# Kernel tuning notes

Hardware: AMD Instinct MI355X
Metric: run time of the kernel (lower is better)

The kernel has to match this reference:

```python
import jax, jax.numpy as jnp
import numpy as np

DIM = 1024
N_HEADS = 16
HEAD_DIM = DIM // N_HEADS
MLP = 4 * DIM
B, N = 2, 2048
LN_EPS = 1e-5


def setup_inputs() -> dict:
    key = jax.random.key(0)
    ks = jax.random.split(key, 12)
    s = lambda fan_in: 1.0 / np.sqrt(fan_in)
    return {
        "x": jax.random.normal(ks[0], (B, N, DIM), dtype=jnp.float32),
        "qkv_w": jax.random.uniform(ks[1], (3 * DIM, DIM), jnp.float32, -s(DIM), s(DIM)),
        "out_w": jax.random.uniform(ks[2], (DIM, DIM), jnp.float32, -s(DIM), s(DIM)),
        "out_b": jax.random.uniform(ks[3], (DIM,), jnp.float32, -s(DIM), s(DIM)),
        "ff_w1": jax.random.uniform(ks[4], (MLP, DIM), jnp.float32, -s(DIM), s(DIM)),
        "ff_b1": jax.random.uniform(ks[5], (MLP,), jnp.float32, -s(DIM), s(DIM)),
        "ff_w2": jax.random.uniform(ks[6], (DIM, MLP), jnp.float32, -s(MLP), s(MLP)),
        "ff_b2": jax.random.uniform(ks[7], (DIM,), jnp.float32, -s(MLP), s(MLP)),
        "ln1_w": jnp.ones((DIM,), jnp.float32),
        "ln1_b": jnp.zeros((DIM,), jnp.float32),
        "ln2_w": jnp.ones((DIM,), jnp.float32),
        "ln2_b": jnp.zeros((DIM,), jnp.float32),
    }


def _layernorm(x, w, b):
    mu = jnp.mean(x, axis=-1, keepdims=True)
    var = jnp.mean(jnp.square(x - mu), axis=-1, keepdims=True)
    return (x - mu) * jax.lax.rsqrt(var + LN_EPS) * w + b


def reference(x, qkv_w, out_w, out_b, ff_w1, ff_b1, ff_w2, ff_b2,
              ln1_w, ln1_b, ln2_w, ln2_b):
    Bx, Nx, D = x.shape
    scale = HEAD_DIM ** -0.5
    x_ln = _layernorm(x, ln1_w, ln1_b)
    qkv = (x_ln @ qkv_w.T).reshape(Bx, Nx, 3, N_HEADS, HEAD_DIM)
    qkv = jnp.transpose(qkv, (2, 0, 3, 1, 4))  # [3, B, H, N, hd]
    q, k, v = qkv[0], qkv[1], qkv[2]
    attn = jnp.einsum('bhid,bhjd->bhij', q, k) * scale
    attn = jax.nn.softmax(attn, axis=-1)
    o = jnp.einsum('bhij,bhjd->bhid', attn, v)
    o = jnp.transpose(o, (0, 2, 1, 3)).reshape(Bx, Nx, D)
    x = x + o @ out_w.T + out_b
    x_ln2 = _layernorm(x, ln2_w, ln2_b)
    h = jax.nn.silu(x_ln2 @ ff_w1.T + ff_b1)
    x = x + h @ ff_w2.T + ff_b2
    return x
```

## Files before the change

### kernel.cpp

```cpp
#include <hip/hip_runtime.h>
#include <stdint.h>

#define DIM   1024
#define NH    16
#define HD    64
#define SEQ   2048
#define BATCH 2
#define MROWS 4096
#define MLPD  4096
#define LN_EPS 1e-5f
#define QSCALE 0.18033688011112042f

typedef _Float16 f16;
typedef _Float16 half8 __attribute__((ext_vector_type(8)));
typedef _Float16 half4 __attribute__((ext_vector_type(4)));
typedef float f32x4 __attribute__((ext_vector_type(4)));

__device__ __forceinline__ void async_cp16(const void* g, void* l) {
  __builtin_amdgcn_global_load_lds(
      (const __attribute__((address_space(1))) unsigned int*)g,
      (__attribute__((address_space(3))) unsigned int*)l, 16, 0, 0);
}

__global__ __launch_bounds__(256) void cvt_all_kernel(
    const float* __restrict__ w0, const float* __restrict__ w1,
    const float* __restrict__ w2, const float* __restrict__ w3,
    f16* __restrict__ d0, f16* __restrict__ d1, f16* __restrict__ d2,
    f16* __restrict__ d3) {
  int blk = blockIdx.x;
  const float* s;
  f16* d;
  int base;
  if (blk < 3072)      { s = w0; d = d0; base = blk; }
  else if (blk < 4096) { s = w1; d = d1; base = blk - 3072; }
  else if (blk < 8192) { s = w2; d = d2; base = blk - 4096; }
  else                 { s = w3; d = d3; base = blk - 8192; }
  int i = (base * 256 + threadIdx.x) * 4;
  float4 v = *(const float4*)(s + i);
  half4 o = { (f16)v.x, (f16)v.y, (f16)v.z, (f16)v.w };
  *(half4*)(d + i) = o;
}

__global__ __launch_bounds__(256) void ln_kernel(const float* __restrict__ x,
    const float* __restrict__ w, const float* __restrict__ b, f16* __restrict__ out) {
  __shared__ float red[8];
  int row = blockIdx.x, t = threadIdx.x;
  const float4 v = ((const float4*)(x + (size_t)row * DIM))[t];
  float s1 = v.x + v.y + v.z + v.w;
  float s2 = v.x * v.x + v.y * v.y + v.z * v.z + v.w * v.w;
#pragma unroll
  for (int m = 32; m; m >>= 1) { s1 += __shfl_xor(s1, m); s2 += __shfl_xor(s2, m); }
  if ((t & 63) == 0) { red[t >> 6] = s1; red[4 + (t >> 6)] = s2; }
  __syncthreads();
  s1 = red[0] + red[1] + red[2] + red[3];
  s2 = red[4] + red[5] + red[6] + red[7];
  float mu = s1 * (1.f / DIM);
  float rs = rsqrtf(s2 * (1.f / DIM) - mu * mu + LN_EPS);
  float4 wv = ((const float4*)w)[t];
  float4 bv = ((const float4*)b)[t];
  half4 o = { (f16)((v.x - mu) * rs * wv.x + bv.x), (f16)((v.y - mu) * rs * wv.y + bv.y),
              (f16)((v.z - mu) * rs * wv.z + bv.z), (f16)((v.w - mu) * rs * wv.w + bv.w) };
  ((half4*)(out + (size_t)row * DIM))[t] = o;
}

template <int MODE, int TN>
__global__ __launch_bounds__(256) void gemm_bt(
    const f16* __restrict__ A, const f16* __restrict__ W,
    const float* __restrict__ bias, const float* __restrict__ resid,
    float* __restrict__ outf, f16* __restrict__ outq, f16* __restrict__ outk,
    f16* __restrict__ outv, int K) {
  constexpr int IT = (TN == 128) ? 4 : 2;
  constexpr int MSUB = IT * 16;
  __shared__ __align__(16) f16 As[128 * 64];
  __shared__ __align__(16) f16 Bs[TN * 64];
  const int t = threadIdx.x;
  const int wave = t >> 6, lane = t & 63;
  const int n16 = lane & 15, quad = lane >> 4;
  const int tile_m = blockIdx.y * 128, tile_n = blockIdx.x * TN;
  const int wm = (TN == 128) ? (wave >> 1) : wave;
  const int wn = (TN == 128) ? (wave & 1) : 0;
  const int srow = lane >> 3, spos = lane & 7;
  const f32x4 zero4 = {0.f, 0.f, 0.f, 0.f};

  f32x4 acc[IT][4];
#pragma unroll
  for (int i = 0; i < IT; i++)
#pragma unroll
    for (int j = 0; j < 4; j++) acc[i][j] = zero4;

  for (int k0 = 0; k0 < K; k0 += 64) {
#pragma unroll
    for (int q = 0; q < 4; q++) {
      int r = q * 32 + wave * 8 + srow;
      int c = spos ^ (r & 7);
      async_cp16(A + (size_t)(tile_m + r) * K + k0 + c * 8, &As[q * 2048 + wave * 512]);
    }
#pragma unroll
    for (int q = 0; q < TN / 32; q++) {
      int r = q * 32 + wave * 8 + srow;
      int c = spos ^ (r & 7);
      async_cp16(W + (size_t)(tile_n + r) * K + k0 + c * 8, &Bs[q * 2048 + wave * 512]);
    }
    __syncthreads();
#pragma unroll
    for (int kk = 0; kk < 2; kk++) {
      half8 af[IT], bfr[4];
#pragma unroll
      for (int i = 0; i < IT; i++) {
        int row = wm * MSUB + i * 16 + n16;
        int c = (kk * 4 + quad) ^ (row & 7);
        af[i] = *(const half8*)&As[row * 64 + c * 8];
      }
#pragma unroll
      for (int j = 0; j < 4; j++) {
        int row = wn * 64 + j * 16 + n16;
        int c = (kk * 4 + quad) ^ (row & 7);
        bfr[j] = *(const half8*)&Bs[row * 64 + c * 8];
      }
#pragma unroll
      for (int i = 0; i < IT; i++)
#pragma unroll
        for (int j = 0; j < 4; j++)
          acc[i][j] = __builtin_amdgcn_mfma_f32_16x16x32_f16(af[i], bfr[j], acc[i][j], 0, 0, 0);
    }
    __syncthreads();
  }

#pragma unroll
  for (int i = 0; i < IT; i++) {
#pragma unroll
    for (int j = 0; j < 4; j++) {
      int gcol = tile_n + wn * 64 + j * 16 + n16;
      int grow0 = tile_m + wm * MSUB + i * 16 + quad * 4;
      if constexpr (MODE == 0) {
        int tsel = gcol >> 10, h = (gcol >> 6) & 15, d = gcol & 63;
        int bb = grow0 >> 11, nn0 = grow0 & 2047;
        if (tsel == 2) {
          half4 o;
#pragma unroll
          for (int r = 0; r < 4; r++) o[r] = (f16)acc[i][j][r];
          *(half4*)&outv[(((size_t)bb * NH + h) * HD + d) * SEQ + nn0] = o;
        } else {
          f16* dst = (tsel == 0) ? outq : outk;
          float sc = (tsel == 0) ? QSCALE : 1.0f;
#pragma unroll
          for (int r = 0; r < 4; r++)
            dst[(((size_t)bb * NH + h) * SEQ + nn0 + r) * HD + d] = (f16)(acc[i][j][r] * sc);
        }
      } else if constexpr (MODE == 1) {
#pragma unroll
        for (int r = 0; r < 4; r++) {
          size_t idx = (size_t)(grow0 + r) * DIM + gcol;
          outf[idx] = acc[i][j][r] + bias[gcol] + resid[idx];
        }
      } else {
#pragma unroll
        for (int r = 0; r < 4; r++) {
          float z = acc[i][j][r] + bias[gcol];
          float sg = 1.f / (1.f + __expf(-z));
          outq[(size_t)(grow0 + r) * MLPD + gcol] = (f16)(z * sg);
        }
      }
    }
  }
}

__global__ __launch_bounds__(256) void attn_kernel(const f16* __restrict__ qg,
    const f16* __restrict__ kg, const f16* __restrict__ vtg, f16* __restrict__ og) {
  __shared__ __align__(16) f16 Ks[64 * 64];
  __shared__ __align__(16) f16 Vs[64 * 64];
  const int bh = blockIdx.y, q0 = blockIdx.x * 64;
  const int t = threadIdx.x, wave = t >> 6, lane = t & 63;
  const int n16 = lane & 15, quad = lane >> 4;
  const int srow = lane >> 3, spos = lane & 7;
  const f32x4 zero4 = {0.f, 0.f, 0.f, 0.f};

  half8 qf0, qf1;
  {
    const f16* qr = qg + ((size_t)bh * SEQ + q0 + wave * 16 + n16) * HD + quad * 8;
    qf0 = *(const half8*)qr;
    qf1 = *(const half8*)(qr + 32);
  }

  f32x4 oc[4];
#pragma unroll
  for (int dt = 0; dt < 4; dt++) oc[dt] = zero4;
  float ls = 0.f;

  for (int kt64 = 0; kt64 < SEQ / 64; kt64++) {
    const int kv0 = kt64 * 64;
#pragma unroll
    for (int p = 0; p < 2; p++) {
      int r = p * 32 + wave * 8 + srow;
      int c = spos ^ (r & 7);
      async_cp16(kg + ((size_t)bh * SEQ + kv0 + r) * HD + c * 8, &Ks[p * 2048 + wave * 512]);
      async_cp16(vtg + ((size_t)bh * HD + r) * SEQ + kv0 + c * 8, &Vs[p * 2048 + wave * 512]);
    }
    __syncthreads();

    half4 pf[4];
#pragma unroll
    for (int kt = 0; kt < 4; kt++) {
      int row = kt * 16 + n16;
      half8 kf0 = *(const half8*)&Ks[row * 64 + (quad ^ (row & 7)) * 8];
      half8 kf1 = *(const half8*)&Ks[row * 64 + ((quad + 4) ^ (row & 7)) * 8];
      f32x4 z = zero4;
      z = __builtin_amdgcn_mfma_f32_16x16x32_f16(kf0, qf0, z, 0, 0, 0);
      z = __builtin_amdgcn_mfma_f32_16x16x32_f16(kf1, qf1, z, 0, 0, 0);
      half4 p4;
#pragma unroll
      for (int r = 0; r < 4; r++) {
        float p = __builtin_exp2f(z[r]);
        ls += p;
        p4[r] = (f16)p;
      }
      pf[kt] = p4;
    }

#pragma unroll
    for (int kt = 0; kt < 4; kt++) {
      half4 va[4];
#pragma unroll
      for (int dt = 0; dt < 4; dt++) {
        int row = dt * 16 + n16;
        int phys = (kt * 2 + (quad >> 1)) ^ (row & 7);
        va[dt] = *(const half4*)&Vs[row * 64 + phys * 8 + (quad & 1) * 4];
      }
#pragma unroll
      for (int dt = 0; dt < 4; dt++)
        oc[dt] = __builtin_amdgcn_mfma_f32_16x16x16f16(va[dt], pf[kt], oc[dt], 0, 0, 0);
    }
    __syncthreads();
  }

  ls += __shfl_xor(ls, 16);
  ls += __shfl_xor(ls, 32);
  float inv = 1.f / ls;
  const int b = bh >> 4, h = bh & 15;
#pragma unroll
  for (int dt = 0; dt < 4; dt++) {
    half4 o;
#pragma unroll
    for (int r = 0; r < 4; r++) o[r] = (f16)(oc[dt][r] * inv);
    *(half4*)&og[((size_t)b * SEQ + q0 + wave * 16 + n16) * DIM + h * HD + dt * 16 + quad * 4] = o;
  }
}

extern "C" void kernel_launch(void* const* d_in, const int* in_sizes, int n_in,
                              void* d_out, int out_size, void* d_ws, size_t ws_size,
                              hipStream_t stream) {
  const float* x     = (const float*)d_in[0];
  const float* qkv_w = (const float*)d_in[1];
  const float* out_w = (const float*)d_in[2];
  const float* out_b = (const float*)d_in[3];
  const float* ff_w1 = (const float*)d_in[4];
  const float* ff_b1 = (const float*)d_in[5];
  const float* ff_w2 = (const float*)d_in[6];
  const float* ff_b2 = (const float*)d_in[7];
  const float* ln1_w = (const float*)d_in[8];
  const float* ln1_b = (const float*)d_in[9];
  const float* ln2_w = (const float*)d_in[10];
  const float* ln2_b = (const float*)d_in[11];
  float* out = (float*)d_out;

  char* p = (char*)d_ws;
  size_t off = 0;
  auto alloc = [&](size_t bytes) {
    void* r = p + off;
    off += (bytes + 255) & ~(size_t)255;
    return r;
  };
  f16* wqkv = (f16*)alloc((size_t)3 * DIM * DIM * 2);
  f16* wout = (f16*)alloc((size_t)DIM * DIM * 2);
  f16* wf1  = (f16*)alloc((size_t)MLPD * DIM * 2);
  f16* wf2  = (f16*)alloc((size_t)MLPD * DIM * 2);
  f16* xln  = (f16*)alloc((size_t)MROWS * DIM * 2);
  f16* qb   = (f16*)alloc((size_t)MROWS * DIM * 2);
  f16* kb   = (f16*)alloc((size_t)MROWS * DIM * 2);
  f16* vtb  = (f16*)alloc((size_t)MROWS * DIM * 2);
  f16* obuf = (f16*)alloc((size_t)MROWS * DIM * 2);
  float* x1 = (float*)alloc((size_t)MROWS * DIM * 4);
  f16* hbuf = (f16*)alloc((size_t)MROWS * MLPD * 2);
  f16* x1ln = xln;

  cvt_all_kernel<<<12288, 256, 0, stream>>>(qkv_w, out_w, ff_w1, ff_w2,
                                            wqkv, wout, wf1, wf2);
  ln_kernel<<<MROWS, 256, 0, stream>>>(x, ln1_w, ln1_b, xln);
  gemm_bt<0, 128><<<dim3(3 * DIM / 128, MROWS / 128), 256, 0, stream>>>(
      xln, wqkv, nullptr, nullptr, nullptr, qb, kb, vtb, DIM);
  attn_kernel<<<dim3(SEQ / 64, BATCH * NH), 256, 0, stream>>>(qb, kb, vtb, obuf);
  gemm_bt<1, 64><<<dim3(DIM / 64, MROWS / 128), 256, 0, stream>>>(
      obuf, wout, out_b, x, x1, nullptr, nullptr, nullptr, DIM);
  ln_kernel<<<MROWS, 256, 0, stream>>>(x1, ln2_w, ln2_b, x1ln);
  gemm_bt<2, 128><<<dim3(MLPD / 128, MROWS / 128), 256, 0, stream>>>(
      x1ln, wf1, ff_b1, nullptr, nullptr, hbuf, nullptr, nullptr, DIM);
  gemm_bt<1, 64><<<dim3(DIM / 64, MROWS / 128), 256, 0, stream>>>(
      hbuf, wf2, ff_b2, x1, out, nullptr, nullptr, nullptr, MLPD);
}
```

Before: 368.7 us.

## Split attention over KV halves with 128-query tiles and a reduction kernel

Each attention block now handles 128 queries, two 16-row query tiles per wave, so every K/V tile loaded into shared memory is reused across twice as many queries. The key sequence is split into two 1024-key chunks along a new grid dimension. Each chunk writes unnormalized fp32 partial outputs and row sums into a scratch area that reuses the MLP hidden buffer, and a new reduce kernel combines the halves and normalizes to fp16. The aim is less K/V load and sync overhead per query while keeping the same block count, at the cost of extra fp32 partial traffic, a second launch and higher register pressure. The partials are summed without max subtraction, which matches the before code's use of exp2 without a running max.

```diff
diff --git a/kernel.cpp b/kernel.cpp
--- a/kernel.cpp
+++ b/kernel.cpp
@@ -165,30 +165,34 @@
   }
 }
 
-__global__ __launch_bounds__(256) void attn_kernel(const f16* __restrict__ qg,
-    const f16* __restrict__ kg, const f16* __restrict__ vtg, f16* __restrict__ og) {
+__global__ __launch_bounds__(256, 4) void attn_kernel(const f16* __restrict__ qg,
+    const f16* __restrict__ kg, const f16* __restrict__ vtg,
+    float* __restrict__ op, float* __restrict__ lp) {
   __shared__ __align__(16) f16 Ks[64 * 64];
   __shared__ __align__(16) f16 Vs[64 * 64];
-  const int bh = blockIdx.y, q0 = blockIdx.x * 64;
+  const int bh = blockIdx.z, kc = blockIdx.y, q0 = blockIdx.x * 128;
   const int t = threadIdx.x, wave = t >> 6, lane = t & 63;
   const int n16 = lane & 15, quad = lane >> 4;
   const int srow = lane >> 3, spos = lane & 7;
   const f32x4 zero4 = {0.f, 0.f, 0.f, 0.f};
 
-  half8 qf0, qf1;
-  {
-    const f16* qr = qg + ((size_t)bh * SEQ + q0 + wave * 16 + n16) * HD + quad * 8;
-    qf0 = *(const half8*)qr;
-    qf1 = *(const half8*)(qr + 32);
-  }
-
-  f32x4 oc[4];
-#pragma unroll
-  for (int dt = 0; dt < 4; dt++) oc[dt] = zero4;
-  float ls = 0.f;
-
-  for (int kt64 = 0; kt64 < SEQ / 64; kt64++) {
-    const int kv0 = kt64 * 64;
+  half8 qf[2][2];
+#pragma unroll
+  for (int qt = 0; qt < 2; qt++) {
+    const f16* qr = qg + ((size_t)bh * SEQ + q0 + wave * 32 + qt * 16 + n16) * HD + quad * 8;
+    qf[qt][0] = *(const half8*)qr;
+    qf[qt][1] = *(const half8*)(qr + 32);
+  }
+
+  f32x4 oc[2][4];
+#pragma unroll
+  for (int qt = 0; qt < 2; qt++)
+#pragma unroll
+    for (int dt = 0; dt < 4; dt++) oc[qt][dt] = zero4;
+  float ls[2] = {0.f, 0.f};
+
+  for (int kt64 = 0; kt64 < 16; kt64++) {
+    const int kv0 = kc * 1024 + kt64 * 64;
 #pragma unroll
     for (int p = 0; p < 2; p++) {
       int r = p * 32 + wave * 8 + srow;
@@ -198,24 +202,35 @@
     }
     __syncthreads();
 
-    half4 pf[4];
+    f32x4 st[4][2];
 #pragma unroll
     for (int kt = 0; kt < 4; kt++) {
       int row = kt * 16 + n16;
       half8 kf0 = *(const half8*)&Ks[row * 64 + (quad ^ (row & 7)) * 8];
       half8 kf1 = *(const half8*)&Ks[row * 64 + ((quad + 4) ^ (row & 7)) * 8];
-      f32x4 z = zero4;
-      z = __builtin_amdgcn_mfma_f32_16x16x32_f16(kf0, qf0, z, 0, 0, 0);
-      z = __builtin_amdgcn_mfma_f32_16x16x32_f16(kf1, qf1, z, 0, 0, 0);
-      half4 p4;
-#pragma unroll
-      for (int r = 0; r < 4; r++) {
-        float p = __builtin_exp2f(z[r]);
-        ls += p;
-        p4[r] = (f16)p;
-      }
-      pf[kt] = p4;
-    }
+#pragma unroll
+      for (int qt = 0; qt < 2; qt++) {
+        f32x4 z = zero4;
+        z = __builtin_amdgcn_mfma_f32_16x16x32_f16(kf0, qf[qt][0], z, 0, 0, 0);
+        z = __builtin_amdgcn_mfma_f32_16x16x32_f16(kf1, qf[qt][1], z, 0, 0, 0);
+        st[kt][qt] = z;
+      }
+    }
+
+    half4 pf[2][4];
+#pragma unroll
+    for (int qt = 0; qt < 2; qt++)
+#pragma unroll
+      for (int kt = 0; kt < 4; kt++) {
+        half4 p4;
+        float s0 = __builtin_exp2f(st[kt][qt][0]);
+        float s1 = __builtin_exp2f(st[kt][qt][1]);
+        float s2 = __builtin_exp2f(st[kt][qt][2]);
+        float s3 = __builtin_exp2f(st[kt][qt][3]);
+        p4[0] = (f16)s0; p4[1] = (f16)s1; p4[2] = (f16)s2; p4[3] = (f16)s3;
+        ls[qt] += (s0 + s1) + (s2 + s3);
+        pf[qt][kt] = p4;
+      }
 
 #pragma unroll
     for (int kt = 0; kt < 4; kt++) {
@@ -228,22 +243,43 @@
       }
 #pragma unroll
       for (int dt = 0; dt < 4; dt++)
-        oc[dt] = __builtin_amdgcn_mfma_f32_16x16x16f16(va[dt], pf[kt], oc[dt], 0, 0, 0);
+#pragma unroll
+        for (int qt = 0; qt < 2; qt++)
+          oc[qt][dt] = __builtin_amdgcn_mfma_f32_16x16x16f16(va[dt], pf[qt][kt], oc[qt][dt], 0, 0, 0);
     }
     __syncthreads();
   }
 
-  ls += __shfl_xor(ls, 16);
-  ls += __shfl_xor(ls, 32);
-  float inv = 1.f / ls;
   const int b = bh >> 4, h = bh & 15;
 #pragma unroll
-  for (int dt = 0; dt < 4; dt++) {
-    half4 o;
-#pragma unroll
-    for (int r = 0; r < 4; r++) o[r] = (f16)(oc[dt][r] * inv);
-    *(half4*)&og[((size_t)b * SEQ + q0 + wave * 16 + n16) * DIM + h * HD + dt * 16 + quad * 4] = o;
-  }
+  for (int qt = 0; qt < 2; qt++) {
+    float l = ls[qt];
+    l += __shfl_xor(l, 16);
+    l += __shfl_xor(l, 32);
+    int q = q0 + wave * 32 + qt * 16 + n16;
+    int row = b * SEQ + q;
+#pragma unroll
+    for (int dt = 0; dt < 4; dt++)
+      *(f32x4*)&op[((size_t)kc * MROWS + row) * DIM + h * HD + dt * 16 + quad * 4] = oc[qt][dt];
+    if (quad == 0) lp[((size_t)kc * BATCH * NH + bh) * SEQ + q] = l;
+  }
+}
+
+__global__ __launch_bounds__(256) void attn_reduce_kernel(const float* __restrict__ op,
+    const float* __restrict__ lp, f16* __restrict__ obuf) {
+  int row = blockIdx.x;
+  int t = threadIdx.x;
+  int b = row >> 11, q = row & 2047;
+  int h = t >> 4;
+  size_t base = (size_t)row * DIM + t * 4;
+  float4 o1 = *(const float4*)&op[base];
+  float4 o2 = *(const float4*)&op[(size_t)MROWS * DIM + base];
+  size_t li = ((size_t)b * NH + h) * SEQ + q;
+  float l = lp[li] + lp[(size_t)BATCH * NH * SEQ + li];
+  float inv = 1.f / l;
+  half4 o = { (f16)((o1.x + o2.x) * inv), (f16)((o1.y + o2.y) * inv),
+              (f16)((o1.z + o2.z) * inv), (f16)((o1.w + o2.w) * inv) };
+  *(half4*)&obuf[base] = o;
 }
 
 extern "C" void kernel_launch(void* const* d_in, const int* in_sizes, int n_in,
@@ -281,14 +317,17 @@
   f16* obuf = (f16*)alloc((size_t)MROWS * DIM * 2);
   float* x1 = (float*)alloc((size_t)MROWS * DIM * 4);
   f16* hbuf = (f16*)alloc((size_t)MROWS * MLPD * 2);
+  float* lp = (float*)alloc((size_t)2 * BATCH * NH * SEQ * 4);
   f16* x1ln = xln;
+  float* op = (float*)hbuf;
 
   cvt_all_kernel<<<12288, 256, 0, stream>>>(qkv_w, out_w, ff_w1, ff_w2,
                                             wqkv, wout, wf1, wf2);
   ln_kernel<<<MROWS, 256, 0, stream>>>(x, ln1_w, ln1_b, xln);
   gemm_bt<0, 128><<<dim3(3 * DIM / 128, MROWS / 128), 256, 0, stream>>>(
       xln, wqkv, nullptr, nullptr, nullptr, qb, kb, vtb, DIM);
-  attn_kernel<<<dim3(SEQ / 64, BATCH * NH), 256, 0, stream>>>(qb, kb, vtb, obuf);
+  attn_kernel<<<dim3(SEQ / 128, 2, BATCH * NH), 256, 0, stream>>>(qb, kb, vtb, op, lp);
+  attn_reduce_kernel<<<MROWS, 256, 0, stream>>>(op, lp, obuf);
   gemm_bt<1, 64><<<dim3(DIM / 64, MROWS / 128), 256, 0, stream>>>(
       obuf, wout, out_b, x, x1, nullptr, nullptr, nullptr, DIM);
   ln_kernel<<<MROWS, 256, 0, stream>>>(x1, ln2_w, ln2_b, x1ln);
```

After: 364.5 us. No clear change (-1.1%).
